# Kernel tuning notes

Measured on AMD Instinct MI355X. Metric: run time of the kernel, lower is better.

Reference implementation:

```python
import jax, jax.numpy as jnp
import numpy as np

N = 100_000   # num nodes
E = 1_600_000 # num edges
C = 128       # in_channels == hidden_channels
L = 3         # n_layers
EPS = 1e-5    # BatchNorm eps (torch default)


def bn(h, g, b, m, v):
    # BatchNorm1d in eval mode: running stats
    return (h - m) * jax.lax.rsqrt(v + EPS) * g + b


def sage_layer(h, src, dst, Wl_i, bl_i, Wr_i):
    # mean aggregation of incoming neighbor messages (PyG SAGEConv default)
    msg = h[src]                                                   # [E, C] gather
    agg = jax.ops.segment_sum(msg, dst, num_segments=N)            # [N, C]
    cnt = jax.ops.segment_sum(jnp.ones((src.shape[0],), h.dtype), dst, num_segments=N)
    agg = agg / jnp.maximum(cnt, 1.0)[:, None]
    return agg @ Wl_i + bl_i + h @ Wr_i                            # lin_l(agg) + lin_r(x)


def setup_inputs() -> dict:
    key = jax.random.key(0)
    ks = jax.random.split(key, 32)
    s = 0.05
    d = {}
    d["x"] = jax.random.normal(ks[0], (N, C), jnp.float32)
    d["edge_index"] = jax.random.randint(ks[1], (2, E), 0, N, dtype=jnp.int32)
    d["batch_size"] = 50_000
    d["Wl"] = jax.random.normal(ks[2], (L, C, C), jnp.float32) * s
    d["bl"] = jax.random.normal(ks[3], (L, C), jnp.float32) * s
    d["Wr"] = jax.random.normal(ks[4], (L, C, C), jnp.float32) * s
    d["bn_g"] = jax.random.uniform(ks[5], (L, C), jnp.float32, 0.5, 1.5)
    d["bn_b"] = jax.random.normal(ks[6], (L, C), jnp.float32) * s
    d["bn_m"] = jax.random.normal(ks[7], (L, C), jnp.float32) * s
    d["bn_v"] = jax.random.uniform(ks[8], (L, C), jnp.float32, 0.5, 1.5)
    d["cW1"] = jax.random.normal(ks[9], (C, C), jnp.float32) * s
    d["cb1"] = jax.random.normal(ks[10], (C,), jnp.float32) * s
    d["cg1"] = jax.random.uniform(ks[11], (C,), jnp.float32, 0.5, 1.5)
    d["cbe1"] = jax.random.normal(ks[12], (C,), jnp.float32) * s
    d["cm1"] = jax.random.normal(ks[13], (C,), jnp.float32) * s
    d["cv1"] = jax.random.uniform(ks[14], (C,), jnp.float32, 0.5, 1.5)
    d["cW2"] = jax.random.normal(ks[15], (C, C // 2), jnp.float32) * s
    d["cb2"] = jax.random.normal(ks[16], (C // 2,), jnp.float32) * s
    d["cg2"] = jax.random.uniform(ks[17], (C // 2,), jnp.float32, 0.5, 1.5)
    d["cbe2"] = jax.random.normal(ks[18], (C // 2,), jnp.float32) * s
    d["cm2"] = jax.random.normal(ks[19], (C // 2,), jnp.float32) * s
    d["cv2"] = jax.random.uniform(ks[20], (C // 2,), jnp.float32, 0.5, 1.5)
    d["cW3"] = jax.random.normal(ks[21], (C // 2, 1), jnp.float32) * s
    d["cb3"] = jax.random.normal(ks[22], (1,), jnp.float32) * s
    return d


def reference(x, edge_index, batch_size, Wl, bl, Wr, bn_g, bn_b, bn_m, bn_v,
              cW1, cb1, cg1, cbe1, cm1, cv1,
              cW2, cb2, cg2, cbe2, cm2, cv2, cW3, cb3):
    src, dst = edge_index[0], edge_index[1]
    h = x
    for l in range(L):  # small fixed layer count
        h = bn(jax.nn.relu(sage_layer(h, src, dst, Wl[l], bl[l], Wr[l])),
               bn_g[l], bn_b[l], bn_m[l], bn_v[l])
        # dropout is identity in eval mode
    h = h[:batch_size]                                             # [B, C] seed nodes
    h = jax.nn.relu(bn(h @ cW1 + cb1, cg1, cbe1, cm1, cv1))
    h = jax.nn.relu(bn(h @ cW2 + cb2, cg2, cbe2, cm2, cv2))
    return (h @ cW3 + cb3)[:, 0]                                   # [B]
```

## Files before the change

### kernel.cpp

```cpp
#include <hip/hip_runtime.h>

#define N_NODES 100000
#define N_EDGES 1600000
#define CDIM    128
#define BATCH   50000
#define NLAYERS 3
#define EPS_BN  1e-5f
#define LPAD    136

#define NBUCK   512
#define BW      196
#define EPB     4096
#define NEB     ((N_EDGES + EPB - 1) / EPB)
#define EBCAP   3584

#define ECAP    704

#define BBLK3   ((BATCH + 31) / 32)

typedef __attribute__((ext_vector_type(8))) short short8;
typedef __attribute__((ext_vector_type(4))) float floatx4;
typedef __attribute__((ext_vector_type(2))) float floatx2;

__device__ __forceinline__ unsigned short f2bf(float f) {
    unsigned int u = __float_as_uint(f);
    u = u + 0x7FFFu + ((u >> 16) & 1u);
    return (unsigned short)(u >> 16);
}
__device__ __forceinline__ unsigned int pk2(float lo, float hi) {
    return (unsigned int)f2bf(lo) | ((unsigned int)f2bf(hi) << 16);
}

__device__ __forceinline__ floatx2 fp8x2_lo(unsigned int u) {
    return __builtin_amdgcn_cvt_pk_f32_fp8((int)u, false);
}
__device__ __forceinline__ floatx2 fp8x2_hi(unsigned int u) {
    return __builtin_amdgcn_cvt_pk_f32_fp8((int)u, true);
}
__device__ __forceinline__ unsigned int f32x4_to_fp8(float f0, float f1, float f2, float f3) {
    int w = __builtin_amdgcn_cvt_pk_fp8_f32(f0, f1, 0, false);
    w = __builtin_amdgcn_cvt_pk_fp8_f32(f2, f3, w, true);
    return (unsigned int)w;
}

__device__ __forceinline__ void acc8(uint2 u, floatx2& a01, floatx2& a23,
                                     floatx2& a45, floatx2& a67) {
    a01 = a01 + fp8x2_lo(u.x);
    a23 = a23 + fp8x2_hi(u.x);
    a45 = a45 + fp8x2_lo(u.y);
    a67 = a67 + fp8x2_hi(u.y);
}
__device__ __forceinline__ void acc8w(uint2 u, float w, floatx2& a01, floatx2& a23,
                                      floatx2& a45, floatx2& a67) {
    floatx2 wv; wv.x = w; wv.y = w;
    a01 = fp8x2_lo(u.x) * wv + a01;
    a23 = fp8x2_hi(u.x) * wv + a23;
    a45 = fp8x2_lo(u.y) * wv + a45;
    a67 = fp8x2_hi(u.y) * wv + a67;
}

#define OFF_HB0   6400000
#define OFF_HB1   12800000
#define OFF_SC    19200000
#define OFF_RP    19201152
#define OFF_BCNT  19301184
#define OFF_ELIST 19302752
#define OFF_EBUF  20902752
#define OFF_WCAT  22737760
#define OFF_WH1   22786912
#define OFF_WH2   22795104
#define OFF_XQ    22800000
#define OFF_HQ0   26000000
#define OFF_HQ1   29200000

#define XBLK 12500
#define WBLK 384
#define HBLK 96
#define SETUP_BLKS (XBLK + WBLK + HBLK + 1)
__global__ __launch_bounds__(256) void setup_fill(
        const float* __restrict__ x,
        const float* __restrict__ Wl, const float* __restrict__ Wr,
        const float* __restrict__ cW1, const float* __restrict__ cW2,
        const float* __restrict__ g, const float* __restrict__ b,
        const float* __restrict__ m, const float* __restrict__ v,
        const float* __restrict__ cg1, const float* __restrict__ cbe1,
        const float* __restrict__ cm1, const float* __restrict__ cv1,
        const float* __restrict__ cg2, const float* __restrict__ cbe2,
        const float* __restrict__ cm2, const float* __restrict__ cv2,
        const int* __restrict__ ei,
        int* __restrict__ bcnt,
        unsigned int* __restrict__ ebuf,
        float* __restrict__ ws) {
    __shared__ unsigned int st[EPB];
    __shared__ unsigned short sb[EPB];
    __shared__ int lh[NBUCK];
    __shared__ int gb[NBUCK];
    __shared__ int lc[NBUCK];

    int blk = blockIdx.x;
    int tid = threadIdx.x;
    unsigned short* xb = (unsigned short*)ws;

    if (blk < XBLK) {
        int i = blk * 256 + tid;
        float4 vv = ((const float4*)x)[i];
        ushort4 o;
        o.x = f2bf(vv.x); o.y = f2bf(vv.y); o.z = f2bf(vv.z); o.w = f2bf(vv.w);
        ((ushort4*)xb)[i] = o;
        unsigned int* xq = (unsigned int*)(ws + OFF_XQ);
        xq[i] = f32x4_to_fp8(vv.x, vv.y, vv.z, vv.w);
        return;
    }
    if (blk < XBLK + WBLK) {
        unsigned short* wcat = (unsigned short*)(ws + OFF_WCAT);
        int i = (blk - XBLK) * 256 + tid;
        int l = i >> 15;
        int n = (i >> 8) & 127;
        int k = i & 255;
        float w = (k < CDIM) ? Wl[((size_t)l * CDIM + k) * CDIM + n]
                             : Wr[((size_t)l * CDIM + (k - CDIM)) * CDIM + n];
        wcat[i] = f2bf(w);
        return;
    }
    if (blk < XBLK + WBLK + HBLK) {
        unsigned short* wh1 = (unsigned short*)(ws + OFF_WH1);
        unsigned short* wh2 = (unsigned short*)(ws + OFF_WH2);
        int i = (blk - XBLK - WBLK) * 256 + tid;
        if (i < 128 * 128) {
            int n = i >> 7, k = i & 127;
            wh1[i] = f2bf(cW1[k * 128 + n]);
        } else if (i < 128 * 128 + 64 * 128) {
            int j = i - 128 * 128;
            int n = j >> 7, k = j & 127;
            wh2[j] = f2bf(cW2[k * 64 + n]);
        }
        return;
    }
    if (blk == XBLK + WBLK + HBLK) {
        float* sc = ws + OFF_SC;
        for (int i = tid; i < NLAYERS * CDIM; i += 256) {
            float s = g[i] * rsqrtf(v[i] + EPS_BN);
            sc[i] = s;
            sc[NLAYERS * CDIM + i] = b[i] - m[i] * s;
        }
        if (tid < CDIM) {
            float s = cg1[tid] * rsqrtf(cv1[tid] + EPS_BN);
            sc[768 + tid] = s;
            sc[896 + tid] = cbe1[tid] - cm1[tid] * s;
        }
        if (tid < 64) {
            float s = cg2[tid] * rsqrtf(cv2[tid] + EPS_BN);
            sc[1024 + tid] = s;
            sc[1088 + tid] = cbe2[tid] - cm2[tid] * s;
        }
        return;
    }

    int fb = blk - SETUP_BLKS;
    for (int t = tid; t < NBUCK; t += 256) { lh[t] = 0; lc[t] = 0; }
    __syncthreads();
    int base = fb * EPB;
    int cnt = min(EPB, N_EDGES - base);
    for (int k = tid; k < cnt / 4; k += 256) {
        int4 s4 = ((const int4*)(ei + base))[k];
        int4 d4 = ((const int4*)(ei + N_EDGES + base))[k];
        int i0 = k * 4;
#pragma unroll
        for (int q = 0; q < 4; ++q) {
            int s = (q == 0) ? s4.x : (q == 1) ? s4.y : (q == 2) ? s4.z : s4.w;
            int d = (q == 0) ? d4.x : (q == 1) ? d4.y : (q == 2) ? d4.z : d4.w;
            int bk = (unsigned)d / BW;
            int ld = d - bk * BW;
            st[i0 + q] = (unsigned)s | ((unsigned)ld << 17);
            sb[i0 + q] = (unsigned short)bk;
            atomicAdd(&lh[bk], 1);
        }
    }
    __syncthreads();
    for (int t = tid; t < NBUCK; t += 256) {
        int c = lh[t];
        gb[t] = c ? (t * EBCAP + atomicAdd(&bcnt[t], c)) : 0;
    }
    __syncthreads();
    for (int i = tid; i < cnt; i += 256) {
        int bk = sb[i];
        int pos = gb[bk] + atomicAdd(&lc[bk], 1);
        ebuf[pos] = st[i];
    }
}

__global__ __launch_bounds__(256) void bucket_csr(const unsigned int* __restrict__ ebuf,
                                                  const int* __restrict__ bcnt,
                                                  int* __restrict__ elist,
                                                  int* __restrict__ rowptr) {
    __shared__ int sbb[NBUCK];
    __shared__ unsigned int st[EBCAP];
    __shared__ int out[EBCAP];
    __shared__ int h[256], sscan[256], pre[256], cur[256];
    int b = blockIdx.x;
    int tid = threadIdx.x;
    int cnt = min(bcnt[b], EBCAP);

    sbb[tid] = bcnt[tid];
    sbb[tid + 256] = bcnt[tid + 256];
    h[tid] = 0; cur[tid] = 0;
    __syncthreads();
    for (int off = 1; off < NBUCK; off <<= 1) {
        int v0 = (tid >= off) ? sbb[tid - off] : 0;
        int t2 = tid + 256;
        int v1 = sbb[t2 - off];
        __syncthreads();
        sbb[tid] += v0;
        sbb[t2] += v1;
        __syncthreads();
    }
    int obase = (b == 0) ? 0 : sbb[b - 1];

    int ebase = b * EBCAP;
    for (int i = tid; i < cnt; i += 256) {
        unsigned int u = ebuf[ebase + i];
        st[i] = u;
        atomicAdd(&h[u >> 17], 1);
    }
    __syncthreads();
    sscan[tid] = h[tid];
    __syncthreads();
    for (int off = 1; off < 256; off <<= 1) {
        int v = (tid >= off) ? sscan[tid - off] : 0;
        __syncthreads();
        sscan[tid] += v;
        __syncthreads();
    }
    pre[tid] = sscan[tid] - h[tid];
    __syncthreads();
    for (int i = tid; i < cnt; i += 256) {
        unsigned int u = st[i];
        int ld = u >> 17;
        int pos = pre[ld] + atomicAdd(&cur[ld], 1);
        out[pos] = (int)(u & 0x1FFFFu);
    }
    __syncthreads();
    for (int i = tid; i < cnt; i += 256) elist[obase + i] = out[i];
    int gn = b * BW + tid;
    if (tid < BW && gn < N_NODES) rowptr[gn] = obase + pre[tid];
    if (b == 0 && tid == 0) rowptr[N_NODES] = N_EDGES;
}

__global__ __launch_bounds__(256, 6) void sage_fused(const int* __restrict__ rowptr,
                                                     const int* __restrict__ elist,
                                                     const unsigned short* __restrict__ hin,
                                                     const unsigned char* __restrict__ hinq,
                                                     unsigned short* __restrict__ hout,
                                                     unsigned char* __restrict__ houtq,
                                                     int wq,
                                                     const unsigned short* __restrict__ wcat,
                                                     const float* __restrict__ bl,
                                                     const float* __restrict__ scale,
                                                     const float* __restrict__ shift) {
    __shared__ unsigned short sA[32][LPAD];
    __shared__ unsigned short sH[32][LPAD];
    __shared__ int selist[ECAP + 8];
    __shared__ int srp[33];

    int row0 = blockIdx.x * 32;
    int tid = threadIdx.x;
    int lane = tid & 31;
    int grp = tid >> 5;
    int sub = lane >> 4;
    int li  = lane & 15;
    int li8 = li * 8;

    int beg0 = rowptr[row0];
    int end0 = rowptr[row0 + 32];
    int ecnt = min(end0 - beg0, ECAP);
    for (int i = tid; i < ecnt + 8; i += 256)
        selist[i] = (i < ecnt) ? elist[beg0 + i] : 0;
    if (tid < 33) srp[tid] = rowptr[row0 + tid];
    for (int it = 0; it < 4; ++it) {
        int idx = it * 256 + tid;
        int r = idx >> 5;
        int c4 = idx & 31;
        uint2 u = ((const uint2*)(hin + (size_t)(row0 + r) * CDIM))[c4];
        *((uint2*)&sH[r][c4 * 4]) = u;
    }
    __syncthreads();

    for (int rr = 0; rr < 4; ++rr) {
        int r = rr * 8 + grp;
        int beg = srp[r];
        int end = srp[r + 1];
        bool all_cached = (end - beg0) <= ecnt;
        floatx2 a01 = (floatx2)0.f, a23 = (floatx2)0.f,
                a45 = (floatx2)0.f, a67 = (floatx2)0.f;

        for (int j = beg + sub * 8; j < end; j += 16) {
            int lj = j - beg0;
            int s0, s1, s2, s3, s4, s5, s6, s7;
            if (all_cached || (lj + 8 <= ecnt)) {
                s0 = selist[lj];     s1 = selist[lj + 1];
                s2 = selist[lj + 2]; s3 = selist[lj + 3];
                s4 = selist[lj + 4]; s5 = selist[lj + 5];
                s6 = selist[lj + 6]; s7 = selist[lj + 7];
            } else {
                s0 = elist[j];     s1 = elist[j + 1];
                s2 = elist[j + 2]; s3 = elist[j + 3];
                s4 = elist[j + 4]; s5 = elist[j + 5];
                s6 = elist[j + 6]; s7 = elist[j + 7];
            }
            bool p1 = (j + 1 < end), p2 = (j + 2 < end), p3 = (j + 3 < end),
                 p4 = (j + 4 < end), p5 = (j + 5 < end), p6 = (j + 6 < end),
                 p7 = (j + 7 < end);
            s1 = p1 ? s1 : 0; s2 = p2 ? s2 : 0; s3 = p3 ? s3 : 0;
            s4 = p4 ? s4 : 0; s5 = p5 ? s5 : 0; s6 = p6 ? s6 : 0;
            s7 = p7 ? s7 : 0;
            uint2 u0 = *((const uint2*)(hinq + (unsigned)((s0 << 7) + li8)));
            uint2 u1 = *((const uint2*)(hinq + (unsigned)((s1 << 7) + li8)));
            uint2 u2 = *((const uint2*)(hinq + (unsigned)((s2 << 7) + li8)));
            uint2 u3 = *((const uint2*)(hinq + (unsigned)((s3 << 7) + li8)));
            uint2 u4 = *((const uint2*)(hinq + (unsigned)((s4 << 7) + li8)));
            uint2 u5 = *((const uint2*)(hinq + (unsigned)((s5 << 7) + li8)));
            uint2 u6 = *((const uint2*)(hinq + (unsigned)((s6 << 7) + li8)));
            uint2 u7 = *((const uint2*)(hinq + (unsigned)((s7 << 7) + li8)));
            acc8(u0, a01, a23, a45, a67);
            acc8w(u1, p1 ? 1.f : 0.f, a01, a23, a45, a67);
            acc8w(u2, p2 ? 1.f : 0.f, a01, a23, a45, a67);
            acc8w(u3, p3 ? 1.f : 0.f, a01, a23, a45, a67);
            acc8w(u4, p4 ? 1.f : 0.f, a01, a23, a45, a67);
            acc8w(u5, p5 ? 1.f : 0.f, a01, a23, a45, a67);
            acc8w(u6, p6 ? 1.f : 0.f, a01, a23, a45, a67);
            acc8w(u7, p7 ? 1.f : 0.f, a01, a23, a45, a67);
        }

        float a0 = a01.x, a1 = a01.y, a2 = a23.x, a3 = a23.y,
              a4 = a45.x, a5 = a45.y, a6 = a67.x, a7 = a67.y;
        a0 += __shfl_xor(a0, 16); a1 += __shfl_xor(a1, 16);
        a2 += __shfl_xor(a2, 16); a3 += __shfl_xor(a3, 16);
        a4 += __shfl_xor(a4, 16); a5 += __shfl_xor(a5, 16);
        a6 += __shfl_xor(a6, 16); a7 += __shfl_xor(a7, 16);
        if (sub == 0) {
            float rin = 1.0f / fmaxf((float)(end - beg), 1.0f);
            uint4 o;
            o.x = pk2(a0 * rin, a1 * rin);
            o.y = pk2(a2 * rin, a3 * rin);
            o.z = pk2(a4 * rin, a5 * rin);
            o.w = pk2(a6 * rin, a7 * rin);
            *((uint4*)&sA[r][li8]) = o;
        }
    }
    __syncthreads();

    int wave = tid >> 6;
    int wl   = tid & 63;
    int ln16 = wl & 15;
    int quad = wl >> 4;

    floatx4 acc[2][2];
#pragma unroll
    for (int mt = 0; mt < 2; ++mt)
#pragma unroll
        for (int nt = 0; nt < 2; ++nt) acc[mt][nt] = (floatx4)0.0f;

    const unsigned short* wbase = wcat + ((size_t)(wave * 32 + ln16) * 256 + quad * 8);

#pragma unroll
    for (int kb = 0; kb < 8; ++kb) {
        int koff = (kb & 3) * 32 + quad * 8;
        const unsigned short* sbuf = (kb < 4) ? &sA[0][0] : &sH[0][0];
        short8 a0 = *((const short8*)(sbuf + (ln16)      * LPAD + koff));
        short8 a1 = *((const short8*)(sbuf + (ln16 + 16) * LPAD + koff));
        short8 b0 = *((const short8*)(wbase + kb * 32));
        short8 b1 = *((const short8*)(wbase + 16 * 256 + kb * 32));
        acc[0][0] = __builtin_amdgcn_mfma_f32_16x16x32_bf16(a0, b0, acc[0][0], 0, 0, 0);
        acc[1][0] = __builtin_amdgcn_mfma_f32_16x16x32_bf16(a1, b0, acc[1][0], 0, 0, 0);
        acc[0][1] = __builtin_amdgcn_mfma_f32_16x16x32_bf16(a0, b1, acc[0][1], 0, 0, 0);
        acc[1][1] = __builtin_amdgcn_mfma_f32_16x16x32_bf16(a1, b1, acc[1][1], 0, 0, 0);
    }

    __syncthreads();
#pragma unroll
    for (int nt = 0; nt < 2; ++nt) {
        int col = wave * 32 + nt * 16 + ln16;
        float bb = bl[col];
        float ss = scale[col];
        float tt = shift[col];
#pragma unroll
        for (int mt = 0; mt < 2; ++mt) {
#pragma unroll
            for (int r = 0; r < 4; ++r) {
                float v = fmaxf(acc[mt][nt][r] + bb, 0.0f) * ss + tt;
                sA[mt * 16 + quad * 4 + r][col] = f2bf(v);
            }
        }
    }
    __syncthreads();
#pragma unroll
    for (int it = 0; it < 2; ++it) {
        int idx = it * 256 + tid;
        int r = idx >> 4;
        int c = idx & 15;
        uint4 u = *((const uint4*)&sA[r][c * 8]);
        *((uint4*)(hout + (size_t)(row0 + r) * CDIM + c * 8)) = u;
        if (wq) {
            float f0 = __uint_as_float(u.x << 16), f1 = __uint_as_float(u.x & 0xFFFF0000u);
            float f2 = __uint_as_float(u.y << 16), f3 = __uint_as_float(u.y & 0xFFFF0000u);
            float f4 = __uint_as_float(u.z << 16), f5 = __uint_as_float(u.z & 0xFFFF0000u);
            float f6 = __uint_as_float(u.w << 16), f7 = __uint_as_float(u.w & 0xFFFF0000u);
            uint2 q;
            q.x = f32x4_to_fp8(f0, f1, f2, f3);
            q.y = f32x4_to_fp8(f4, f5, f6, f7);
            *((uint2*)(houtq + (size_t)(row0 + r) * 128 + c * 8)) = q;
        }
    }
}

__global__ __launch_bounds__(256, 4) void head_fused(const unsigned short* __restrict__ hin,
                                                     const unsigned short* __restrict__ wh1,
                                                     const unsigned short* __restrict__ wh2,
                                                     const float* __restrict__ cb1,
                                                     const float* __restrict__ s1,
                                                     const float* __restrict__ t1,
                                                     const float* __restrict__ cb2,
                                                     const float* __restrict__ s2,
                                                     const float* __restrict__ t2,
                                                     const float* __restrict__ W3,
                                                     const float* __restrict__ b3,
                                                     float* __restrict__ out) {
    __shared__ unsigned short sZ[64][LPAD];
    __shared__ float sP[4][64];
    __shared__ float sw3[64];

    int row0 = blockIdx.x * 64;
    int tid = threadIdx.x;
    if (tid < 64) sw3[tid] = W3[tid];

    for (int it = 0; it < 4; ++it) {
        int idx = it * 256 + tid;
        int r = idx >> 4;
        int c = idx & 15;
        uint4 u = *((const uint4*)(hin + (size_t)(row0 + r) * CDIM + c * 8));
        *((uint4*)&sZ[r][c * 8]) = u;
    }
    __syncthreads();

    int wave = tid >> 6;
    int wl   = tid & 63;
    int ln16 = wl & 15;
    int quad = wl >> 4;

    floatx4 a1[4][2];
#pragma unroll
    for (int mt = 0; mt < 4; ++mt) { a1[mt][0] = (floatx4)0.0f; a1[mt][1] = (floatx4)0.0f; }

    const unsigned short* w1a = wh1 + (size_t)(wave * 32 + ln16) * 128 + quad * 8;
    const unsigned short* w1b = w1a + 16 * 128;

#pragma unroll
    for (int kb = 0; kb < 4; ++kb) {
        int koff = kb * 32 + quad * 8;
        short8 b0 = *((const short8*)(w1a + kb * 32));
        short8 b1 = *((const short8*)(w1b + kb * 32));
#pragma unroll
        for (int mt = 0; mt < 4; ++mt) {
            short8 af = *((const short8*)(&sZ[mt * 16 + ln16][koff]));
            a1[mt][0] = __builtin_amdgcn_mfma_f32_16x16x32_bf16(af, b0, a1[mt][0], 0, 0, 0);
            a1[mt][1] = __builtin_amdgcn_mfma_f32_16x16x32_bf16(af, b1, a1[mt][1], 0, 0, 0);
        }
    }

    __syncthreads();
#pragma unroll
    for (int nt = 0; nt < 2; ++nt) {
        int col = wave * 32 + nt * 16 + ln16;
        float bb = cb1[col], ss = s1[col], tt = t1[col];
#pragma unroll
        for (int mt = 0; mt < 4; ++mt) {
#pragma unroll
            for (int r = 0; r < 4; ++r) {
                float v = fmaxf((a1[mt][nt][r] + bb) * ss + tt, 0.0f);
                sZ[mt * 16 + quad * 4 + r][col] = f2bf(v);
            }
        }
    }
    __syncthreads();

    floatx4 a2[4];
#pragma unroll
    for (int mt = 0; mt < 4; ++mt) a2[mt] = (floatx4)0.0f;

    const unsigned short* w2a = wh2 + (size_t)(wave * 16 + ln16) * 128 + quad * 8;

#pragma unroll
    for (int kb = 0; kb < 4; ++kb) {
        int koff = kb * 32 + quad * 8;
        short8 b0 = *((const short8*)(w2a + kb * 32));
#pragma unroll
        for (int mt = 0; mt < 4; ++mt) {
            short8 af = *((const short8*)(&sZ[mt * 16 + ln16][koff]));
            a2[mt] = __builtin_amdgcn_mfma_f32_16x16x32_bf16(af, b0, a2[mt], 0, 0, 0);
        }
    }

    {
        int col = wave * 16 + ln16;
        float bb = cb2[col], ss = s2[col], tt = t2[col];
        float w3v = sw3[col];
#pragma unroll
        for (int mt = 0; mt < 4; ++mt) {
#pragma unroll
            for (int r = 0; r < 4; ++r) {
                float v = fmaxf((a2[mt][r] + bb) * ss + tt, 0.0f) * w3v;
                v += __shfl_xor(v, 1);
                v += __shfl_xor(v, 2);
                v += __shfl_xor(v, 4);
                v += __shfl_xor(v, 8);
                if (ln16 == 0) sP[wave][mt * 16 + quad * 4 + r] = v;
            }
        }
    }
    __syncthreads();
    if (tid < 64) {
        int row = row0 + tid;
        if (row < BATCH)
            out[row] = sP[0][tid] + sP[1][tid] + sP[2][tid] + sP[3][tid] + b3[0];
    }
}

extern "C" void kernel_launch(void* const* d_in, const int* in_sizes, int n_in,
                              void* d_out, int out_size, void* d_ws, size_t ws_size,
                              hipStream_t stream) {
    const float* x    = (const float*)d_in[0];
    const int*   ei   = (const int*)d_in[1];
    const float* Wl   = (const float*)d_in[3];
    const float* bl   = (const float*)d_in[4];
    const float* Wr   = (const float*)d_in[5];
    const float* bn_g = (const float*)d_in[6];
    const float* bn_b = (const float*)d_in[7];
    const float* bn_m = (const float*)d_in[8];
    const float* bn_v = (const float*)d_in[9];
    const float* cW1  = (const float*)d_in[10];
    const float* cb1  = (const float*)d_in[11];
    const float* cg1  = (const float*)d_in[12];
    const float* cbe1 = (const float*)d_in[13];
    const float* cm1  = (const float*)d_in[14];
    const float* cv1  = (const float*)d_in[15];
    const float* cW2  = (const float*)d_in[16];
    const float* cb2  = (const float*)d_in[17];
    const float* cg2  = (const float*)d_in[18];
    const float* cbe2 = (const float*)d_in[19];
    const float* cm2  = (const float*)d_in[20];
    const float* cv2  = (const float*)d_in[21];
    const float* cW3  = (const float*)d_in[22];
    const float* cb3  = (const float*)d_in[23];

    float* ws  = (float*)d_ws;
    unsigned short* xb  = (unsigned short*)ws;
    unsigned short* hb0 = (unsigned short*)(ws + OFF_HB0);
    unsigned short* hb1 = (unsigned short*)(ws + OFF_HB1);
    float* sc    = ws + OFF_SC;
    int* rowptr  = (int*)(ws + OFF_RP);
    int* bcnt    = (int*)(ws + OFF_BCNT);
    int* elist   = (int*)(ws + OFF_ELIST);
    unsigned int* ebuf = (unsigned int*)(ws + OFF_EBUF);
    unsigned short* wcat = (unsigned short*)(ws + OFF_WCAT);
    unsigned short* wh1  = (unsigned short*)(ws + OFF_WH1);
    unsigned short* wh2  = (unsigned short*)(ws + OFF_WH2);
    unsigned char* xq  = (unsigned char*)(ws + OFF_XQ);
    unsigned char* hq0 = (unsigned char*)(ws + OFF_HQ0);
    unsigned char* hq1 = (unsigned char*)(ws + OFF_HQ1);

    hipMemsetAsync(bcnt, 0, NBUCK * sizeof(int), stream);

    setup_fill<<<SETUP_BLKS + NEB, 256, 0, stream>>>(
        x, Wl, Wr, cW1, cW2,
        bn_g, bn_b, bn_m, bn_v,
        cg1, cbe1, cm1, cv1,
        cg2, cbe2, cm2, cv2,
        ei, bcnt, ebuf, ws);

    bucket_csr<<<NBUCK, 256, 0, stream>>>(ebuf, bcnt, elist, rowptr);

    const unsigned short* lin[NLAYERS]  = { xb, hb0, hb1 };
    const unsigned char*  linq[NLAYERS] = { xq, hq0, hq1 };
    unsigned short* lout[NLAYERS]       = { hb0, hb1, hb0 };
    unsigned char*  loutq[NLAYERS]      = { hq0, hq1, hq0 };
    int wqf[NLAYERS]   = { 1, 1, 0 };
    int grids[NLAYERS] = { N_NODES / 32, N_NODES / 32, BBLK3 };
    for (int l = 0; l < NLAYERS; ++l) {
        sage_fused<<<grids[l], 256, 0, stream>>>(
            rowptr, elist, lin[l], linq[l], lout[l], loutq[l], wqf[l],
            wcat + (size_t)l * CDIM * 256,
            bl + (size_t)l * CDIM,
            sc + l * CDIM, sc + 384 + l * CDIM);
    }

    head_fused<<<(BATCH + 63) / 64, 256, 0, stream>>>(
        hb0, wh1, wh2,
        cb1, sc + 768, sc + 896,
        cb2, sc + 1024, sc + 1088,
        cW3, cb3, (float*)d_out);
}
```

Baseline: 331.9 us.

## Fuse classifier head into last SAGE layer and read self features from global

The separate head kernel is removed and its two MFMA GEMMs, BN/ReLU and the final dot product now run inside the third sage_fused launch, operating on the 32-row tile still held in shared memory. This skips writing the layer-3 output to global memory and reading it back. The self-feature (sH) staging buffer is dropped and those MFMA operands are loaded straight from global memory, which frees LDS and lets the launch bound rise from 6 to 8 blocks per SM. The trade-off is uncoalesced global loads in the MFMA loop and tighter register limits from the higher occupancy target.

```diff
diff --git a/kernel.cpp b/kernel.cpp
--- a/kernel.cpp
+++ b/kernel.cpp
@@ -246,7 +246,7 @@
     if (b == 0 && tid == 0) rowptr[N_NODES] = N_EDGES;
 }
 
-__global__ __launch_bounds__(256, 6) void sage_fused(const int* __restrict__ rowptr,
+__global__ __launch_bounds__(256, 8) void sage_fused(const int* __restrict__ rowptr,
                                                      const int* __restrict__ elist,
                                                      const unsigned short* __restrict__ hin,
                                                      const unsigned char* __restrict__ hinq,
@@ -256,11 +256,23 @@
                                                      const unsigned short* __restrict__ wcat,
                                                      const float* __restrict__ bl,
                                                      const float* __restrict__ scale,
-                                                     const float* __restrict__ shift) {
+                                                     const float* __restrict__ shift,
+                                                     const unsigned short* __restrict__ wh1,
+                                                     const unsigned short* __restrict__ wh2,
+                                                     const float* __restrict__ cb1,
+                                                     const float* __restrict__ s1,
+                                                     const float* __restrict__ t1,
+                                                     const float* __restrict__ cb2,
+                                                     const float* __restrict__ s2,
+                                                     const float* __restrict__ t2,
+                                                     const float* __restrict__ W3,
+                                                     const float* __restrict__ b3,
+                                                     float* __restrict__ out) {
     __shared__ unsigned short sA[32][LPAD];
-    __shared__ unsigned short sH[32][LPAD];
     __shared__ int selist[ECAP + 8];
     __shared__ int srp[33];
+    __shared__ float sP[4][32];
+    __shared__ float sw3[64];
 
     int row0 = blockIdx.x * 32;
     int tid = threadIdx.x;
@@ -276,13 +288,7 @@
     for (int i = tid; i < ecnt + 8; i += 256)
         selist[i] = (i < ecnt) ? elist[beg0 + i] : 0;
     if (tid < 33) srp[tid] = rowptr[row0 + tid];
-    for (int it = 0; it < 4; ++it) {
-        int idx = it * 256 + tid;
-        int r = idx >> 5;
-        int c4 = idx & 31;
-        uint2 u = ((const uint2*)(hin + (size_t)(row0 + r) * CDIM))[c4];
-        *((uint2*)&sH[r][c4 * 4]) = u;
-    }
+    if (out && tid < 64) sw3[tid] = W3[tid];
     __syncthreads();
 
     for (int rr = 0; rr < 4; ++rr) {
@@ -295,32 +301,32 @@
 
         for (int j = beg + sub * 8; j < end; j += 16) {
             int lj = j - beg0;
-            int s0, s1, s2, s3, s4, s5, s6, s7;
+            int s0, s1q, s2q, s3q, s4q, s5q, s6q, s7q;
             if (all_cached || (lj + 8 <= ecnt)) {
-                s0 = selist[lj];     s1 = selist[lj + 1];
-                s2 = selist[lj + 2]; s3 = selist[lj + 3];
-                s4 = selist[lj + 4]; s5 = selist[lj + 5];
-                s6 = selist[lj + 6]; s7 = selist[lj + 7];
+                s0  = selist[lj];     s1q = selist[lj + 1];
+                s2q = selist[lj + 2]; s3q = selist[lj + 3];
+                s4q = selist[lj + 4]; s5q = selist[lj + 5];
+                s6q = selist[lj + 6]; s7q = selist[lj + 7];
             } else {
-                s0 = elist[j];     s1 = elist[j + 1];
-                s2 = elist[j + 2]; s3 = elist[j + 3];
-                s4 = elist[j + 4]; s5 = elist[j + 5];
-                s6 = elist[j + 6]; s7 = elist[j + 7];
+                s0  = elist[j];     s1q = elist[j + 1];
+                s2q = elist[j + 2]; s3q = elist[j + 3];
+                s4q = elist[j + 4]; s5q = elist[j + 5];
+                s6q = elist[j + 6]; s7q = elist[j + 7];
             }
             bool p1 = (j + 1 < end), p2 = (j + 2 < end), p3 = (j + 3 < end),
                  p4 = (j + 4 < end), p5 = (j + 5 < end), p6 = (j + 6 < end),
                  p7 = (j + 7 < end);
-            s1 = p1 ? s1 : 0; s2 = p2 ? s2 : 0; s3 = p3 ? s3 : 0;
-            s4 = p4 ? s4 : 0; s5 = p5 ? s5 : 0; s6 = p6 ? s6 : 0;
-            s7 = p7 ? s7 : 0;
-            uint2 u0 = *((const uint2*)(hinq + (unsigned)((s0 << 7) + li8)));
-            uint2 u1 = *((const uint2*)(hinq + (unsigned)((s1 << 7) + li8)));
-            uint2 u2 = *((const uint2*)(hinq + (unsigned)((s2 << 7) + li8)));
-            uint2 u3 = *((const uint2*)(hinq + (unsigned)((s3 << 7) + li8)));
-            uint2 u4 = *((const uint2*)(hinq + (unsigned)((s4 << 7) + li8)));
-            uint2 u5 = *((const uint2*)(hinq + (unsigned)((s5 << 7) + li8)));
-            uint2 u6 = *((const uint2*)(hinq + (unsigned)((s6 << 7) + li8)));
-            uint2 u7 = *((const uint2*)(hinq + (unsigned)((s7 << 7) + li8)));
+            s1q = p1 ? s1q : 0; s2q = p2 ? s2q : 0; s3q = p3 ? s3q : 0;
+            s4q = p4 ? s4q : 0; s5q = p5 ? s5q : 0; s6q = p6 ? s6q : 0;
+            s7q = p7 ? s7q : 0;
+            uint2 u0 = *((const uint2*)(hinq + (unsigned)((s0  << 7) + li8)));
+            uint2 u1 = *((const uint2*)(hinq + (unsigned)((s1q << 7) + li8)));
+            uint2 u2 = *((const uint2*)(hinq + (unsigned)((s2q << 7) + li8)));
+            uint2 u3 = *((const uint2*)(hinq + (unsigned)((s3q << 7) + li8)));
+            uint2 u4 = *((const uint2*)(hinq + (unsigned)((s4q << 7) + li8)));
+            uint2 u5 = *((const uint2*)(hinq + (unsigned)((s5q << 7) + li8)));
+            uint2 u6 = *((const uint2*)(hinq + (unsigned)((s6q << 7) + li8)));
+            uint2 u7 = *((const uint2*)(hinq + (unsigned)((s7q << 7) + li8)));
             acc8(u0, a01, a23, a45, a67);
             acc8w(u1, p1 ? 1.f : 0.f, a01, a23, a45, a67);
             acc8w(u2, p2 ? 1.f : 0.f, a01, a23, a45, a67);
@@ -361,13 +367,14 @@
         for (int nt = 0; nt < 2; ++nt) acc[mt][nt] = (floatx4)0.0f;
 
     const unsigned short* wbase = wcat + ((size_t)(wave * 32 + ln16) * 256 + quad * 8);
-
-#pragma unroll
-    for (int kb = 0; kb < 8; ++kb) {
-        int koff = (kb & 3) * 32 + quad * 8;
-        const unsigned short* sbuf = (kb < 4) ? &sA[0][0] : &sH[0][0];
-        short8 a0 = *((const short8*)(sbuf + (ln16)      * LPAD + koff));
-        short8 a1 = *((const short8*)(sbuf + (ln16 + 16) * LPAD + koff));
+    const unsigned short* hr0 = hin + (size_t)(row0 + ln16) * CDIM;
+    const unsigned short* hr1 = hin + (size_t)(row0 + 16 + ln16) * CDIM;
+
+#pragma unroll
+    for (int kb = 0; kb < 4; ++kb) {
+        int koff = kb * 32 + quad * 8;
+        short8 a0 = *((const short8*)(&sA[ln16][koff]));
+        short8 a1 = *((const short8*)(&sA[ln16 + 16][koff]));
         short8 b0 = *((const short8*)(wbase + kb * 32));
         short8 b1 = *((const short8*)(wbase + 16 * 256 + kb * 32));
         acc[0][0] = __builtin_amdgcn_mfma_f32_16x16x32_bf16(a0, b0, acc[0][0], 0, 0, 0);
@@ -375,6 +382,18 @@
         acc[0][1] = __builtin_amdgcn_mfma_f32_16x16x32_bf16(a0, b1, acc[0][1], 0, 0, 0);
         acc[1][1] = __builtin_amdgcn_mfma_f32_16x16x32_bf16(a1, b1, acc[1][1], 0, 0, 0);
     }
+#pragma unroll
+    for (int kb = 4; kb < 8; ++kb) {
+        int koff = (kb - 4) * 32 + quad * 8;
+        short8 a0 = *((const short8*)(hr0 + koff));
+        short8 a1 = *((const short8*)(hr1 + koff));
+        short8 b0 = *((const short8*)(wbase + kb * 32));
+        short8 b1 = *((const short8*)(wbase + 16 * 256 + kb * 32));
+        acc[0][0] = __builtin_amdgcn_mfma_f32_16x16x32_bf16(a0, b0, acc[0][0], 0, 0, 0);
+        acc[1][0] = __builtin_amdgcn_mfma_f32_16x16x32_bf16(a1, b0, acc[1][0], 0, 0, 0);
+        acc[0][1] = __builtin_amdgcn_mfma_f32_16x16x32_bf16(a0, b1, acc[0][1], 0, 0, 0);
+        acc[1][1] = __builtin_amdgcn_mfma_f32_16x16x32_bf16(a1, b1, acc[1][1], 0, 0, 0);
+    }
 
     __syncthreads();
 #pragma unroll
@@ -393,122 +412,84 @@
         }
     }
     __syncthreads();
-#pragma unroll
-    for (int it = 0; it < 2; ++it) {
-        int idx = it * 256 + tid;
-        int r = idx >> 4;
-        int c = idx & 15;
-        uint4 u = *((const uint4*)&sA[r][c * 8]);
-        *((uint4*)(hout + (size_t)(row0 + r) * CDIM + c * 8)) = u;
-        if (wq) {
-            float f0 = __uint_as_float(u.x << 16), f1 = __uint_as_float(u.x & 0xFFFF0000u);
-            float f2 = __uint_as_float(u.y << 16), f3 = __uint_as_float(u.y & 0xFFFF0000u);
-            float f4 = __uint_as_float(u.z << 16), f5 = __uint_as_float(u.z & 0xFFFF0000u);
-            float f6 = __uint_as_float(u.w << 16), f7 = __uint_as_float(u.w & 0xFFFF0000u);
-            uint2 q;
-            q.x = f32x4_to_fp8(f0, f1, f2, f3);
-            q.y = f32x4_to_fp8(f4, f5, f6, f7);
-            *((uint2*)(houtq + (size_t)(row0 + r) * 128 + c * 8)) = q;
-        }
-    }
-}
-
-__global__ __launch_bounds__(256, 4) void head_fused(const unsigned short* __restrict__ hin,
-                                                     const unsigned short* __restrict__ wh1,
-                                                     const unsigned short* __restrict__ wh2,
-                                                     const float* __restrict__ cb1,
-                                                     const float* __restrict__ s1,
-                                                     const float* __restrict__ t1,
-                                                     const float* __restrict__ cb2,
-                                                     const float* __restrict__ s2,
-                                                     const float* __restrict__ t2,
-                                                     const float* __restrict__ W3,
-                                                     const float* __restrict__ b3,
-                                                     float* __restrict__ out) {
-    __shared__ unsigned short sZ[64][LPAD];
-    __shared__ float sP[4][64];
-    __shared__ float sw3[64];
-
-    int row0 = blockIdx.x * 64;
-    int tid = threadIdx.x;
-    if (tid < 64) sw3[tid] = W3[tid];
-
-    for (int it = 0; it < 4; ++it) {
-        int idx = it * 256 + tid;
-        int r = idx >> 4;
-        int c = idx & 15;
-        uint4 u = *((const uint4*)(hin + (size_t)(row0 + r) * CDIM + c * 8));
-        *((uint4*)&sZ[r][c * 8]) = u;
-    }
-    __syncthreads();
-
-    int wave = tid >> 6;
-    int wl   = tid & 63;
-    int ln16 = wl & 15;
-    int quad = wl >> 4;
-
-    floatx4 a1[4][2];
-#pragma unroll
-    for (int mt = 0; mt < 4; ++mt) { a1[mt][0] = (floatx4)0.0f; a1[mt][1] = (floatx4)0.0f; }
-
+
+    if (!out) {
+#pragma unroll
+        for (int it = 0; it < 2; ++it) {
+            int idx = it * 256 + tid;
+            int r = idx >> 4;
+            int c = idx & 15;
+            uint4 u = *((const uint4*)&sA[r][c * 8]);
+            *((uint4*)(hout + (size_t)(row0 + r) * CDIM + c * 8)) = u;
+            if (wq) {
+                float f0 = __uint_as_float(u.x << 16), f1 = __uint_as_float(u.x & 0xFFFF0000u);
+                float f2 = __uint_as_float(u.y << 16), f3 = __uint_as_float(u.y & 0xFFFF0000u);
+                float f4 = __uint_as_float(u.z << 16), f5 = __uint_as_float(u.z & 0xFFFF0000u);
+                float f6 = __uint_as_float(u.w << 16), f7 = __uint_as_float(u.w & 0xFFFF0000u);
+                uint2 q;
+                q.x = f32x4_to_fp8(f0, f1, f2, f3);
+                q.y = f32x4_to_fp8(f4, f5, f6, f7);
+                *((uint2*)(houtq + (size_t)(row0 + r) * 128 + c * 8)) = q;
+            }
+        }
+        return;
+    }
+
+    floatx4 h1[2][2];
+#pragma unroll
+    for (int mt = 0; mt < 2; ++mt) { h1[mt][0] = (floatx4)0.0f; h1[mt][1] = (floatx4)0.0f; }
     const unsigned short* w1a = wh1 + (size_t)(wave * 32 + ln16) * 128 + quad * 8;
     const unsigned short* w1b = w1a + 16 * 128;
-
 #pragma unroll
     for (int kb = 0; kb < 4; ++kb) {
         int koff = kb * 32 + quad * 8;
         short8 b0 = *((const short8*)(w1a + kb * 32));
         short8 b1 = *((const short8*)(w1b + kb * 32));
 #pragma unroll
-        for (int mt = 0; mt < 4; ++mt) {
-            short8 af = *((const short8*)(&sZ[mt * 16 + ln16][koff]));
-            a1[mt][0] = __builtin_amdgcn_mfma_f32_16x16x32_bf16(af, b0, a1[mt][0], 0, 0, 0);
-            a1[mt][1] = __builtin_amdgcn_mfma_f32_16x16x32_bf16(af, b1, a1[mt][1], 0, 0, 0);
-        }
-    }
-
+        for (int mt = 0; mt < 2; ++mt) {
+            short8 af = *((const short8*)(&sA[mt * 16 + ln16][koff]));
+            h1[mt][0] = __builtin_amdgcn_mfma_f32_16x16x32_bf16(af, b0, h1[mt][0], 0, 0, 0);
+            h1[mt][1] = __builtin_amdgcn_mfma_f32_16x16x32_bf16(af, b1, h1[mt][1], 0, 0, 0);
+        }
+    }
     __syncthreads();
 #pragma unroll
     for (int nt = 0; nt < 2; ++nt) {
         int col = wave * 32 + nt * 16 + ln16;
         float bb = cb1[col], ss = s1[col], tt = t1[col];
 #pragma unroll
-        for (int mt = 0; mt < 4; ++mt) {
+        for (int mt = 0; mt < 2; ++mt) {
 #pragma unroll
             for (int r = 0; r < 4; ++r) {
-                float v = fmaxf((a1[mt][nt][r] + bb) * ss + tt, 0.0f);
-                sZ[mt * 16 + quad * 4 + r][col] = f2bf(v);
+                float v = fmaxf((h1[mt][nt][r] + bb) * ss + tt, 0.0f);
+                sA[mt * 16 + quad * 4 + r][col] = f2bf(v);
             }
         }
     }
     __syncthreads();
 
-    floatx4 a2[4];
-#pragma unroll
-    for (int mt = 0; mt < 4; ++mt) a2[mt] = (floatx4)0.0f;
-
+    floatx4 h2[2];
+    h2[0] = (floatx4)0.0f; h2[1] = (floatx4)0.0f;
     const unsigned short* w2a = wh2 + (size_t)(wave * 16 + ln16) * 128 + quad * 8;
-
 #pragma unroll
     for (int kb = 0; kb < 4; ++kb) {
         int koff = kb * 32 + quad * 8;
         short8 b0 = *((const short8*)(w2a + kb * 32));
 #pragma unroll
-        for (int mt = 0; mt < 4; ++mt) {
-            short8 af = *((const short8*)(&sZ[mt * 16 + ln16][koff]));
-            a2[mt] = __builtin_amdgcn_mfma_f32_16x16x32_bf16(af, b0, a2[mt], 0, 0, 0);
-        }
-    }
-
+        for (int mt = 0; mt < 2; ++mt) {
+            short8 af = *((const short8*)(&sA[mt * 16 + ln16][koff]));
+            h2[mt] = __builtin_amdgcn_mfma_f32_16x16x32_bf16(af, b0, h2[mt], 0, 0, 0);
+        }
+    }
     {
         int col = wave * 16 + ln16;
         float bb = cb2[col], ss = s2[col], tt = t2[col];
         float w3v = sw3[col];
 #pragma unroll
-        for (int mt = 0; mt < 4; ++mt) {
+        for (int mt = 0; mt < 2; ++mt) {
 #pragma unroll
             for (int r = 0; r < 4; ++r) {
-                float v = fmaxf((a2[mt][r] + bb) * ss + tt, 0.0f) * w3v;
+                float v = fmaxf((h2[mt][r] + bb) * ss + tt, 0.0f) * w3v;
                 v += __shfl_xor(v, 1);
                 v += __shfl_xor(v, 2);
                 v += __shfl_xor(v, 4);
@@ -518,7 +499,7 @@
         }
     }
     __syncthreads();
-    if (tid < 64) {
+    if (tid < 32) {
         int row = row0 + tid;
         if (row < BATCH)
             out[row] = sP[0][tid] + sP[1][tid] + sP[2][tid] + sP[3][tid] + b3[0];
@@ -579,22 +560,20 @@
 
     bucket_csr<<<NBUCK, 256, 0, stream>>>(ebuf, bcnt, elist, rowptr);
 
-    const unsigned short* lin[NLAYERS]  = { xb, hb0, hb1 };
-    const unsigned char*  linq[NLAYERS] = { xq, hq0, hq1 };
-    unsigned short* lout[NLAYERS]       = { hb0, hb1, hb0 };
-    unsigned char*  loutq[NLAYERS]      = { hq0, hq1, hq0 };
-    int wqf[NLAYERS]   = { 1, 1, 0 };
-    int grids[NLAYERS] = { N_NODES / 32, N_NODES / 32, BBLK3 };
-    for (int l = 0; l < NLAYERS; ++l) {
-        sage_fused<<<grids[l], 256, 0, stream>>>(
-            rowptr, elist, lin[l], linq[l], lout[l], loutq[l], wqf[l],
-            wcat + (size_t)l * CDIM * 256,
-            bl + (size_t)l * CDIM,
-            sc + l * CDIM, sc + 384 + l * CDIM);
-    }
-
-    head_fused<<<(BATCH + 63) / 64, 256, 0, stream>>>(
-        hb0, wh1, wh2,
+    sage_fused<<<N_NODES / 32, 256, 0, stream>>>(
+        rowptr, elist, xb, xq, hb0, hq0, 1,
+        wcat, bl, sc, sc + 384,
+        nullptr, nullptr, nullptr, nullptr, nullptr,
+        nullptr, nullptr, nullptr, nullptr, nullptr, nullptr);
+    sage_fused<<<N_NODES / 32, 256, 0, stream>>>(
+        rowptr, elist, hb0, hq0, hb1, hq1, 1,
+        wcat + (size_t)CDIM * 256, bl + CDIM, sc + CDIM, sc + 384 + CDIM,
+        nullptr, nullptr, nullptr, nullptr, nullptr,
+        nullptr, nullptr, nullptr, nullptr, nullptr, nullptr);
+    sage_fused<<<BBLK3, 256, 0, stream>>>(
+        rowptr, elist, hb1, hq1, hb0, hq0, 0,
+        wcat + (size_t)2 * CDIM * 256, bl + 2 * CDIM, sc + 2 * CDIM, sc + 384 + 2 * CDIM,
+        wh1, wh2,
         cb1, sc + 768, sc + 896,
         cb2, sc + 1024, sc + 1088,
         cW3, cb3, (float*)d_out);
```

Measured after the change: 350.7 us. 5.7% more time.
